# Performance work log

Measured on AMD Instinct MI355X. Metric: run time of the kernel, lower is better.

## Reference

```python
import jax, jax.numpy as jnp
import numpy as np

N_HEAD = 8
EPS_LN = 1e-5
EPS_SM = 1e-16


def _mlp(x, w1, b1, g, beta, w2, b2):
    # Linear -> ReLU -> LayerNorm -> Linear (matches nn.Sequential in torch module)
    h = jax.nn.relu(x @ w1 + b1)
    mu = jnp.mean(h, axis=-1, keepdims=True)
    var = jnp.mean((h - mu) ** 2, axis=-1, keepdims=True)
    h = (h - mu) * jax.lax.rsqrt(var + EPS_LN) * g + beta
    return h @ w2 + b2


def setup_inputs() -> dict:
    B, L, D, E, Fe, H = 4, 4096, 128, 262144, 5, N_HEAD
    ks = jax.random.split(jax.random.key(0), 20)
    s = 0.02
    p = lambda i, sh: jax.random.normal(ks[i], sh, jnp.float32) * s
    z = lambda n: jnp.zeros((n,), jnp.float32)
    inp = {
        "key": jax.random.normal(ks[0], (B, L, D), jnp.float32),
        "value": jax.random.normal(ks[1], (B, L, D), jnp.float32),
        "query": jax.random.normal(ks[2], (B, L, D), jnp.float32),
        "edge_feats": jax.random.normal(ks[3], (E, Fe), jnp.float32),
        "atten_masks": jnp.zeros((E,), jnp.float32),  # present in signature, unused in forward
        "batch_indices": jax.random.randint(ks[4], (E,), 0, B),
        "head_indices": jax.random.randint(ks[5], (E,), 0, L),
        "tail_indices": jax.random.randint(ks[6], (E,), 0, L),
        "key_w": p(7, (D, D)), "key_b": z(D),
        "query_w": p(8, (D, D)), "query_b": z(D),
        "value_w": p(9, (D, D)), "value_b": z(D),
        "proj_w": p(10, (D, D)), "proj_b": z(D),
        "ea_w1": p(11, (Fe, D)), "ea_b1": z(D), "ea_g": jnp.ones((D,), jnp.float32), "ea_beta": z(D), "ea_w2": p(12, (D, H)), "ea_b2": z(H),
        "ek_w1": p(13, (Fe, D)), "ek_b1": z(D), "ek_g": jnp.ones((D,), jnp.float32), "ek_beta": z(D), "ek_w2": p(14, (D, D)), "ek_b2": z(D),
        "ev_w1": p(15, (Fe, D)), "ev_b1": z(D), "ev_g": jnp.ones((D,), jnp.float32), "ev_beta": z(D), "ev_w2": p(16, (D, D)), "ev_b2": z(D),
    }
    return inp


def reference(key, value, query, edge_feats, atten_masks,
              batch_indices, head_indices, tail_indices,
              key_w, key_b, query_w, query_b, value_w, value_b, proj_w, proj_b,
              ea_w1, ea_b1, ea_g, ea_beta, ea_w2, ea_b2,
              ek_w1, ek_b1, ek_g, ek_beta, ek_w2, ek_b2,
              ev_w1, ev_b1, ev_g, ev_beta, ev_w2, ev_b2):
    B, L, D = query.shape
    H = N_HEAD
    dh = D // H
    N = B * L
    # node projections -> [B*L, H, dh]
    k = (key @ key_w + key_b).reshape(N, H, dh)
    q = (query @ query_w + query_b).reshape(N, H, dh)
    v = (value @ value_w + value_b).reshape(N, H, dh)
    heads = batch_indices * L + head_indices  # destination node per edge
    tails = batch_indices * L + tail_indices  # source node per edge
    # per-edge gather + edge-conditioned k/v
    qs = q[heads]
    ks = k[tails] + _mlp(edge_feats, ek_w1, ek_b1, ek_g, ek_beta, ek_w2, ek_b2).reshape(-1, H, dh)
    vs = v[tails] + _mlp(edge_feats, ev_w1, ev_b1, ev_g, ev_beta, ev_w2, ev_b2).reshape(-1, H, dh)
    w = jnp.sum(ks * qs, axis=-1) + _mlp(edge_feats, ea_w1, ea_b1, ea_g, ea_beta, ea_w2, ea_b2)  # [E, H]
    # segment softmax over edges grouped by destination node
    m = jax.ops.segment_max(w, heads, num_segments=N)
    ex = jnp.exp(w - m[heads])
    denom = jax.ops.segment_sum(ex, heads, num_segments=N)
    att = ex / (denom[heads] + EPS_SM)  # [E, H]
    # weighted scatter-sum combine
    y = jax.ops.segment_sum(att[:, :, None] * vs, heads, num_segments=N).reshape(B, L, D)
    return y @ proj_w + proj_b
```

## Files before the change

### kernel.cpp

```cpp
#include <hip/hip_runtime.h>
#include <hip/hip_bf16.h>

#define D      128
#define NHEAD  8
#define FE     5
#define LSEQ   4096
#define EPB    64
#define NNODE  16384
#define EPS_LN 1e-5f
#define EPS_SM 1e-16f

typedef unsigned short ushort_t;
typedef __bf16 bf16x8 __attribute__((ext_vector_type(8)));
typedef float  f32x4  __attribute__((ext_vector_type(4)));

__device__ __forceinline__ ushort_t f2bf(float x) {
    __hip_bfloat16 b = __float2bfloat16(x);
    return __builtin_bit_cast(unsigned short, b);
}
__device__ __forceinline__ float bf2f(ushort_t u) {
    __hip_bfloat16 b = __builtin_bit_cast(__hip_bfloat16, u);
    return __bfloat162float(b);
}
__device__ __forceinline__ float i2f(int x)  { return __builtin_bit_cast(float, x); }
__device__ __forceinline__ int   f2i(float x){ return __builtin_bit_cast(int, x); }

union Pk8 { ushort_t u[8]; uint4 v; };

__global__ __launch_bounds__(256) void pre_kernel(
    const float* __restrict__ ekw2, const float* __restrict__ evw2,
    const float* __restrict__ eaw2,
    const float* __restrict__ kw, const float* __restrict__ qw,
    const float* __restrict__ vw,
    ushort_t* __restrict__ eksw, ushort_t* __restrict__ evsw, ushort_t* __restrict__ easw,
    ushort_t* __restrict__ kwsw, ushort_t* __restrict__ qwsw, ushort_t* __restrict__ vwsw,
    const int* __restrict__ bidx, const int* __restrict__ hidx,
    int* __restrict__ cnt, int E)
{
    const int t = threadIdx.x;
    if (blockIdx.x < 41) {
        const int g = blockIdx.x * 256 + t;
        const float* src; ushort_t* dst; int frag, ncols = 128, nvalid = 128;
        if (g < 2048)       { src = ekw2; dst = eksw; frag = g; }
        else if (g < 4096)  { src = evw2; dst = evsw; frag = g - 2048; }
        else if (g < 4352)  { src = eaw2; dst = easw; frag = g - 4096; ncols = 8; nvalid = 8; }
        else if (g < 6400)  { src = kw;   dst = kwsw; frag = g - 4352; }
        else if (g < 8448)  { src = qw;   dst = qwsw; frag = g - 6400; }
        else if (g < 10496) { src = vw;   dst = vwsw; frag = g - 8448; }
        else return;
        const int s = (frag >> 6) & 3;
        const int l = frag & 63;
        const int n = ((frag >> 8) << 4) + (l & 15);
        Pk8 pk;
        #pragma unroll
        for (int j = 0; j < 8; ++j) {
            const int k = s * 32 + (l >> 4) * 8 + j;
            const float v = (n < nvalid) ? src[k * ncols + n] : 0.f;
            pk.u[j] = f2bf(v);
        }
        *(uint4*)(dst + (size_t)frag * 8) = pk.v;
        return;
    }
    const int e = (blockIdx.x - 41) * 256 + t;
    if (e < E) atomicAdd(&cnt[bidx[e] * LSEQ + hidx[e]], 1);
}

__global__ __launch_bounds__(1024) void scan16k(
    const int* __restrict__ cnt, int* __restrict__ base)
{
    __shared__ int part[1024];
    const int t = threadIdx.x;
    int v[16], ex[16], s = 0;
    #pragma unroll
    for (int i = 0; i < 16; ++i) v[i] = cnt[t * 16 + i];
    #pragma unroll
    for (int i = 0; i < 16; ++i) { ex[i] = s; s += v[i]; }
    part[t] = s;
    __syncthreads();
    for (int off = 1; off < 1024; off <<= 1) {
        const int x = (t >= off) ? part[t - off] : 0;
        __syncthreads();
        part[t] += x;
        __syncthreads();
    }
    const int boff = (t > 0) ? part[t - 1] : 0;
    #pragma unroll
    for (int i = 0; i < 16; ++i) base[t * 16 + i] = boff + ex[i];
    if (t == 1023) base[NNODE] = boff + s;
}

__global__ __launch_bounds__(256) void mid_kernel(
    const float* __restrict__ key, const float* __restrict__ value,
    const float* __restrict__ query,
    const float* __restrict__ key_b, const float* __restrict__ value_b,
    const float* __restrict__ query_b,
    const ushort_t* __restrict__ kwsw, const ushort_t* __restrict__ vwsw,
    const ushort_t* __restrict__ qwsw,
    ushort_t* __restrict__ k16, ushort_t* __restrict__ v16, ushort_t* __restrict__ q16,
    const int* __restrict__ bidx, const int* __restrict__ hidx, const int* __restrict__ tidx,
    const float* __restrict__ edge_feats,
    const int* __restrict__ base, int* __restrict__ cnt, float* __restrict__ rec,
    int nqm, int E)
{
    const int t  = threadIdx.x;
    const int nq = 3 * nqm;
    if ((int)blockIdx.x < nq) {
        const int which = blockIdx.x / nqm;
        const int blk   = blockIdx.x % nqm;
        const float* X     = (which == 0) ? key   : (which == 1) ? value   : query;
        const float* bias  = (which == 0) ? key_b : (which == 1) ? value_b : query_b;
        const ushort_t* Ww = (which == 0) ? kwsw  : (which == 1) ? vwsw    : qwsw;
        ushort_t* Y        = (which == 0) ? k16   : (which == 1) ? v16     : q16;

        const int mt    = t >> 6;
        const int l     = t & 63;
        const int rbase = blk * 64 + mt * 16;
        const int colb  = l & 15;
        const int row0  = (l >> 4) * 4;
        const int arow  = rbase + colb;
        const int koff  = (l >> 4) * 8;

        bf16x8 afr[4];
        #pragma unroll
        for (int s = 0; s < 4; ++s) {
            const float4 x0 = *(const float4*)&X[(size_t)arow * D + s * 32 + koff];
            const float4 x1 = *(const float4*)&X[(size_t)arow * D + s * 32 + koff + 4];
            Pk8 p8;
            p8.u[0] = f2bf(x0.x); p8.u[1] = f2bf(x0.y);
            p8.u[2] = f2bf(x0.z); p8.u[3] = f2bf(x0.w);
            p8.u[4] = f2bf(x1.x); p8.u[5] = f2bf(x1.y);
            p8.u[6] = f2bf(x1.z); p8.u[7] = f2bf(x1.w);
            afr[s] = __builtin_bit_cast(bf16x8, p8.v);
        }
        #pragma unroll
        for (int nt = 0; nt < 8; ++nt) {
            f32x4 acc = {0.f, 0.f, 0.f, 0.f};
            #pragma unroll
            for (int s = 0; s < 4; ++s) {
                const bf16x8 bfr = *(const bf16x8*)(Ww + (size_t)((nt * 4 + s) * 64 + l) * 8);
                acc = __builtin_amdgcn_mfma_f32_16x16x32_bf16(afr[s], bfr, acc, 0, 0, 0);
            }
            const int col = nt * 16 + colb;
            const float b = bias[col];
            #pragma unroll
            for (int r = 0; r < 4; ++r)
                Y[(size_t)(rbase + row0 + r) * D + col] = f2bf(acc[r] + b);
        }
        return;
    }

    const int e = (blockIdx.x - nq) * 256 + t;
    if (e >= E) return;
    const int bb = bidx[e];
    const int nh = bb * LSEQ + hidx[e];
    const int nt = bb * LSEQ + tidx[e];
    const int slot = atomicSub(&cnt[nh], 1) - 1;
    const int p = base[nh] + slot;
    float ef[FE];
    #pragma unroll
    for (int f = 0; f < FE; ++f) ef[f] = edge_feats[(size_t)e * FE + f];
    *(float4*)&rec[(size_t)p * 8]     = float4{ef[0], ef[1], ef[2], ef[3]};
    *(float4*)&rec[(size_t)p * 8 + 4] = float4{ef[4], i2f(nh), i2f(nt), 0.f};
}

__global__ __launch_bounds__(256, 4) void edge_kernel(
    const float* __restrict__ rec,
    const float* __restrict__ ea_w1, const float* __restrict__ ea_b1,
    const float* __restrict__ ea_g,  const float* __restrict__ ea_be, const float* __restrict__ ea_b2,
    const float* __restrict__ ek_w1, const float* __restrict__ ek_b1,
    const float* __restrict__ ek_g,  const float* __restrict__ ek_be, const float* __restrict__ ek_b2,
    const float* __restrict__ ev_w1, const float* __restrict__ ev_b1,
    const float* __restrict__ ev_g,  const float* __restrict__ ev_be, const float* __restrict__ ev_b2,
    const ushort_t* __restrict__ easw, const ushort_t* __restrict__ eksw, const ushort_t* __restrict__ evsw,
    const ushort_t* __restrict__ k16, const ushort_t* __restrict__ q16, const ushort_t* __restrict__ v16,
    float* __restrict__ ex_ws, ushort_t* __restrict__ vs_ws)
{
    __shared__ float pw1[3][FE * D];
    __shared__ float pb1[3][D], pg[3][D], pbe[3][D];
    __shared__ float pb2k[D], pb2v[D], pb2a[NHEAD];
    __shared__ float ef_s[EPB][FE];
    __shared__ int   eh_s[EPB], et_s[EPB];

    const int t   = threadIdx.x;
    const int e0g = blockIdx.x * EPB;

    for (int i = t; i < FE * D; i += 256) { pw1[0][i] = ea_w1[i]; pw1[1][i] = ek_w1[i]; pw1[2][i] = ev_w1[i]; }
    if (t < D) {
        pb1[0][t] = ea_b1[t]; pb1[1][t] = ek_b1[t]; pb1[2][t] = ev_b1[t];
        pg [0][t] = ea_g [t]; pg [1][t] = ek_g [t]; pg [2][t] = ev_g [t];
        pbe[0][t] = ea_be[t]; pbe[1][t] = ek_be[t]; pbe[2][t] = ev_be[t];
        pb2k[t] = ek_b2[t];   pb2v[t] = ev_b2[t];
        if (t < NHEAD) pb2a[t] = ea_b2[t];
    }
    if (t < 128) {
        const int pl = t >> 1, half = t & 1;
        const float4 v = *(const float4*)&rec[((size_t)e0g + pl) * 8 + half * 4];
        if (half == 0) {
            ef_s[pl][0] = v.x; ef_s[pl][1] = v.y; ef_s[pl][2] = v.z; ef_s[pl][3] = v.w;
        } else {
            ef_s[pl][4] = v.x; eh_s[pl] = f2i(v.y); et_s[pl] = f2i(v.z);
        }
    }
    __syncthreads();

    const int mt   = t >> 6;
    const int l    = t & 63;
    const int qt   = l & 3;
    const int per  = l >> 2;
    const int row0 = (l >> 4) * 4;
    const int colb = l & 15;
    const int src  = 4 * colb + (l >> 4);
    const int bsrc = (l & 48);

    int tn[4], hnn[4];
    #pragma unroll
    for (int r = 0; r < 4; ++r) { tn[r] = et_s[mt*16 + row0 + r]; hnn[r] = eh_s[mt*16 + row0 + r]; }

    float efr[FE];
    #pragma unroll
    for (int f = 0; f < FE; ++f) efr[f] = ef_s[mt*16 + per][f];

    auto first_layer = [&](int m, uint4 pk[4]) {
        const float4* w1v = (const float4*)&pw1[m][0];
        const float4* b1v = (const float4*)&pb1[m][0];
        const float4* gv  = (const float4*)&pg[m][0];
        const float4* bev = (const float4*)&pbe[m][0];
        float4 hv[4][2];
        float s1 = 0.f, s2 = 0.f;
        #pragma unroll
        for (int s = 0; s < 4; ++s) {
            #pragma unroll
            for (int hc = 0; hc < 2; ++hc) {
                const int idx = s * 8 + qt * 2 + hc;
                float4 a = b1v[idx];
                #pragma unroll
                for (int f = 0; f < FE; ++f) {
                    const float sc = efr[f];
                    const float4 w = w1v[f * 32 + idx];
                    a.x = fmaf(sc, w.x, a.x); a.y = fmaf(sc, w.y, a.y);
                    a.z = fmaf(sc, w.z, a.z); a.w = fmaf(sc, w.w, a.w);
                }
                a.x = fmaxf(a.x, 0.f); a.y = fmaxf(a.y, 0.f);
                a.z = fmaxf(a.z, 0.f); a.w = fmaxf(a.w, 0.f);
                hv[s][hc] = a;
                s1 += a.x + a.y + a.z + a.w;
                s2 += a.x*a.x + a.y*a.y + a.z*a.z + a.w*a.w;
            }
        }
        s1 += __shfl_xor(s1, 1); s1 += __shfl_xor(s1, 2);
        s2 += __shfl_xor(s2, 1); s2 += __shfl_xor(s2, 2);
        const float mu = s1 * (1.f / 128.f);
        const float rs = rsqrtf(s2 * (1.f / 128.f) - mu * mu + EPS_LN);
        #pragma unroll
        for (int s = 0; s < 4; ++s) {
            const int idx = s * 8 + qt * 2;
            const float4 x0 = hv[s][0], x1 = hv[s][1];
            const float4 g0 = gv[idx], g1 = gv[idx + 1];
            const float4 b0 = bev[idx], b1 = bev[idx + 1];
            Pk8 p8;
            p8.u[0] = f2bf(fmaf((x0.x - mu) * rs, g0.x, b0.x));
            p8.u[1] = f2bf(fmaf((x0.y - mu) * rs, g0.y, b0.y));
            p8.u[2] = f2bf(fmaf((x0.z - mu) * rs, g0.z, b0.z));
            p8.u[3] = f2bf(fmaf((x0.w - mu) * rs, g0.w, b0.w));
            p8.u[4] = f2bf(fmaf((x1.x - mu) * rs, g1.x, b1.x));
            p8.u[5] = f2bf(fmaf((x1.y - mu) * rs, g1.y, b1.y));
            p8.u[6] = f2bf(fmaf((x1.z - mu) * rs, g1.z, b1.z));
            p8.u[7] = f2bf(fmaf((x1.w - mu) * rs, g1.w, b1.w));
            pk[s] = p8.v;
        }
    };

    auto gather_afr = [&](const uint4 pk[4], bf16x8 afr[4]) {
        #pragma unroll
        for (int s = 0; s < 4; ++s) {
            uint4 w;
            w.x = (unsigned)__shfl((int)pk[s].x, src);
            w.y = (unsigned)__shfl((int)pk[s].y, src);
            w.z = (unsigned)__shfl((int)pk[s].z, src);
            w.w = (unsigned)__shfl((int)pk[s].w, src);
            afr[s] = __builtin_bit_cast(bf16x8, w);
        }
    };

    uint4 pk[4];
    bf16x8 afr[4];

    float eaacc[4];
    first_layer(0, pk);
    gather_afr(pk, afr);
    {
        f32x4 acc = {0.f, 0.f, 0.f, 0.f};
        #pragma unroll
        for (int s = 0; s < 4; ++s) {
            const bf16x8 bfr = *(const bf16x8*)(easw + (size_t)(s * 64 + l) * 8);
            acc = __builtin_amdgcn_mfma_f32_16x16x32_bf16(afr[s], bfr, acc, 0, 0, 0);
        }
        #pragma unroll
        for (int r = 0; r < 4; ++r) eaacc[r] = acc[r];
    }

    first_layer(1, pk);
    gather_afr(pk, afr);
    #pragma unroll
    for (int nt = 0; nt < NHEAD; ++nt) {
        f32x4 acc = {0.f, 0.f, 0.f, 0.f};
        #pragma unroll
        for (int s = 0; s < 4; ++s) {
            const bf16x8 bfr = *(const bf16x8*)(eksw + (size_t)((nt * 4 + s) * 64 + l) * 8);
            acc = __builtin_amdgcn_mfma_f32_16x16x32_bf16(afr[s], bfr, acc, 0, 0, 0);
        }
        const int col = nt * 16 + colb;
        const float b2 = pb2k[col];
        const float ba = pb2a[nt];
        float pr[4];
        #pragma unroll
        for (int r = 0; r < 4; ++r)
            pr[r] = (acc[r] + b2 + bf2f(k16[(size_t)tn[r] * D + col]))
                    * bf2f(q16[(size_t)hnn[r] * D + col]);
        #pragma unroll
        for (int m = 1; m < 16; m <<= 1) {
            #pragma unroll
            for (int r = 0; r < 4; ++r) pr[r] += __shfl_xor(pr[r], m);
        }
        #pragma unroll
        for (int r = 0; r < 4; ++r) {
            const float ea = __shfl(eaacc[r], bsrc | nt);
            const float ex = __expf(pr[r] + ea + ba);
            if (colb == nt)
                ex_ws[(size_t)(e0g + mt*16 + row0 + r) * NHEAD + nt] = ex;
        }
    }

    first_layer(2, pk);
    gather_afr(pk, afr);
    #pragma unroll
    for (int nt = 0; nt < NHEAD; ++nt) {
        f32x4 acc = {0.f, 0.f, 0.f, 0.f};
        #pragma unroll
        for (int s = 0; s < 4; ++s) {
            const bf16x8 bfr = *(const bf16x8*)(evsw + (size_t)((nt * 4 + s) * 64 + l) * 8);
            acc = __builtin_amdgcn_mfma_f32_16x16x32_bf16(afr[s], bfr, acc, 0, 0, 0);
        }
        const int col = nt * 16 + colb;
        const float b2 = pb2v[col];
        #pragma unroll
        for (int r = 0; r < 4; ++r) {
            const float vs = acc[r] + b2 + bf2f(v16[(size_t)tn[r] * D + col]);
            vs_ws[(size_t)(e0g + mt*16 + row0 + r) * D + col] = f2bf(vs);
        }
    }
}

__global__ __launch_bounds__(512) void agg_out(
    const int* __restrict__ base,
    const float* __restrict__ ex_ws, const ushort_t* __restrict__ vs_ws,
    const float* __restrict__ W, const float* __restrict__ bias,
    float* __restrict__ out)
{
    __shared__ float xs[D][20];
    const int t  = threadIdx.x;
    const int rg = t >> 7;
    const int j  = t & 127;
    const int h  = j >> 4;
    const int n0 = blockIdx.x * 16;

    #pragma unroll
    for (int ni = 0; ni < 4; ++ni) {
        const int n  = n0 + rg * 4 + ni;
        const int s0 = base[n], s1 = base[n + 1];
        float acc = 0.f, den = 0.f;
        int p = s0;
        for (; p + 4 <= s1; p += 4) {
            float ex4[4], vs4[4];
            #pragma unroll
            for (int r = 0; r < 4; ++r) {
                ex4[r] = ex_ws[(size_t)(p + r) * NHEAD + h];
                vs4[r] = bf2f(vs_ws[(size_t)(p + r) * D + j]);
            }
            #pragma unroll
            for (int r = 0; r < 4; ++r) {
                den += ex4[r];
                acc = fmaf(ex4[r], vs4[r], acc);
            }
        }
        for (; p < s1; ++p) {
            const float ex = ex_ws[(size_t)p * NHEAD + h];
            den += ex;
            acc = fmaf(ex, bf2f(vs_ws[(size_t)p * D + j]), acc);
        }
        xs[j][rg * 4 + ni] = acc / (den + EPS_SM);
    }
    __syncthreads();

    float acc[4];
    const float b = bias[j];
    #pragma unroll
    for (int r = 0; r < 4; ++r) acc[r] = b;
    #pragma unroll 4
    for (int i = 0; i < D; ++i) {
        const float w = W[i * D + j];
        const float4 y4 = *(const float4*)&xs[i][rg * 4];
        acc[0] = fmaf(y4.x, w, acc[0]); acc[1] = fmaf(y4.y, w, acc[1]);
        acc[2] = fmaf(y4.z, w, acc[2]); acc[3] = fmaf(y4.w, w, acc[3]);
    }
    #pragma unroll
    for (int r = 0; r < 4; ++r)
        out[(size_t)(n0 + rg * 4 + r) * D + j] = acc[r];
}

extern "C" void kernel_launch(void* const* d_in, const int* in_sizes, int n_in,
                              void* d_out, int out_size, void* d_ws, size_t ws_size,
                              hipStream_t stream)
{
    const float* key        = (const float*)d_in[0];
    const float* value      = (const float*)d_in[1];
    const float* query      = (const float*)d_in[2];
    const float* edge_feats = (const float*)d_in[3];
    const int*   bidx       = (const int*)d_in[5];
    const int*   hidx       = (const int*)d_in[6];
    const int*   tidx       = (const int*)d_in[7];
    const float* key_w   = (const float*)d_in[8];  const float* key_b   = (const float*)d_in[9];
    const float* query_w = (const float*)d_in[10]; const float* query_b = (const float*)d_in[11];
    const float* value_w = (const float*)d_in[12]; const float* value_b = (const float*)d_in[13];
    const float* proj_w  = (const float*)d_in[14]; const float* proj_b  = (const float*)d_in[15];

    const int N = in_sizes[0] / D;
    const int E = in_sizes[5];

    char* ws = (char*)d_ws;
    ushort_t* k16   = (ushort_t*)ws; ws += (size_t)N * D * 2;
    ushort_t* q16   = (ushort_t*)ws; ws += (size_t)N * D * 2;
    ushort_t* v16   = (ushort_t*)ws; ws += (size_t)N * D * 2;
    float* ex_ws    = (float*)ws;    ws += (size_t)E * NHEAD * 4;
    ushort_t* vs_ws = (ushort_t*)ws; ws += (size_t)E * D * 2;
    float* rec      = (float*)ws;    ws += (size_t)E * 8 * 4;
    ushort_t* eksw  = (ushort_t*)ws; ws += (size_t)2048 * 8 * 2;
    ushort_t* evsw  = (ushort_t*)ws; ws += (size_t)2048 * 8 * 2;
    ushort_t* easw  = (ushort_t*)ws; ws += (size_t)256 * 8 * 2;
    ushort_t* kwsw  = (ushort_t*)ws; ws += (size_t)2048 * 8 * 2;
    ushort_t* qwsw  = (ushort_t*)ws; ws += (size_t)2048 * 8 * 2;
    ushort_t* vwsw  = (ushort_t*)ws; ws += (size_t)2048 * 8 * 2;
    int* base = (int*)ws;  ws += (size_t)(N + 1) * 4;
    int* cnt  = (int*)ws;  ws += (size_t)N * 4;

    const int nqm   = N / 64;
    const int nhist = (E + 255) / 256;

    hipMemsetAsync(cnt, 0, (size_t)N * 4, stream);

    pre_kernel<<<41 + nhist, 256, 0, stream>>>(
        (const float*)d_in[26], (const float*)d_in[32], (const float*)d_in[20],
        key_w, query_w, value_w,
        eksw, evsw, easw, kwsw, qwsw, vwsw,
        bidx, hidx, cnt, E);

    scan16k<<<1, 1024, 0, stream>>>(cnt, base);

    mid_kernel<<<3 * nqm + nhist, 256, 0, stream>>>(
        key, value, query,
        key_b, value_b, query_b,
        kwsw, vwsw, qwsw,
        k16, v16, q16,
        bidx, hidx, tidx, edge_feats,
        base, cnt, rec, nqm, E);

    edge_kernel<<<E / EPB, 256, 0, stream>>>(
        rec,
        (const float*)d_in[16], (const float*)d_in[17], (const float*)d_in[18],
        (const float*)d_in[19], (const float*)d_in[21],
        (const float*)d_in[22], (const float*)d_in[23], (const float*)d_in[24],
        (const float*)d_in[25], (const float*)d_in[27],
        (const float*)d_in[28], (const float*)d_in[29], (const float*)d_in[30],
        (const float*)d_in[31], (const float*)d_in[33],
        easw, eksw, evsw,
        k16, q16, v16,
        ex_ws, vs_ws);

    agg_out<<<N / 16, 512, 0, stream>>>(base, ex_ws, vs_ws, proj_w, proj_b, (float*)d_out);
}
```

Measured before the change: 296.2 us.

## Compute edge MLP first layer with split-bf16 MFMA instead of scalar FMAs

The first Linear layer of the three edge MLPs (5 inputs to 128 neurons plus bias) moves from per-thread fp32 FMA loops over shared-memory weights to MFMA 16x16x32 bf16 ops. Weights are pre-swizzled in pre_kernel into hi/lo bf16 pairs, with the bias folded in through constant-one inputs, which keeps near-fp32 accuracy. The LayerNorm output is now staged through a padded shared-memory tile to form the A fragments for the second layer, replacing the shuffle-based gather. It frees VALU work and shared memory for weights, at the cost of an extra LDS round trip and a small pre-processing step.

```diff
diff --git a/kernel.cpp b/kernel.cpp
--- a/kernel.cpp
+++ b/kernel.cpp
@@ -32,36 +32,66 @@
     const float* __restrict__ eaw2,
     const float* __restrict__ kw, const float* __restrict__ qw,
     const float* __restrict__ vw,
+    const float* __restrict__ eaw1, const float* __restrict__ eab1,
+    const float* __restrict__ ekw1, const float* __restrict__ ekb1,
+    const float* __restrict__ evw1, const float* __restrict__ evb1,
     ushort_t* __restrict__ eksw, ushort_t* __restrict__ evsw, ushort_t* __restrict__ easw,
     ushort_t* __restrict__ kwsw, ushort_t* __restrict__ qwsw, ushort_t* __restrict__ vwsw,
+    ushort_t* __restrict__ w1fg,
     const int* __restrict__ bidx, const int* __restrict__ hidx,
     int* __restrict__ cnt, int E)
 {
     const int t = threadIdx.x;
-    if (blockIdx.x < 41) {
+    if (blockIdx.x < 47) {
         const int g = blockIdx.x * 256 + t;
-        const float* src; ushort_t* dst; int frag, ncols = 128, nvalid = 128;
-        if (g < 2048)       { src = ekw2; dst = eksw; frag = g; }
-        else if (g < 4096)  { src = evw2; dst = evsw; frag = g - 2048; }
-        else if (g < 4352)  { src = eaw2; dst = easw; frag = g - 4096; ncols = 8; nvalid = 8; }
-        else if (g < 6400)  { src = kw;   dst = kwsw; frag = g - 4352; }
-        else if (g < 8448)  { src = qw;   dst = qwsw; frag = g - 6400; }
-        else if (g < 10496) { src = vw;   dst = vwsw; frag = g - 8448; }
-        else return;
-        const int s = (frag >> 6) & 3;
-        const int l = frag & 63;
-        const int n = ((frag >> 8) << 4) + (l & 15);
+        if (g < 10496) {
+            const float* src; ushort_t* dst; int frag, ncols = 128, nvalid = 128;
+            if (g < 2048)       { src = ekw2; dst = eksw; frag = g; }
+            else if (g < 4096)  { src = evw2; dst = evsw; frag = g - 2048; }
+            else if (g < 4352)  { src = eaw2; dst = easw; frag = g - 4096; ncols = 8; nvalid = 8; }
+            else if (g < 6400)  { src = kw;   dst = kwsw; frag = g - 4352; }
+            else if (g < 8448)  { src = qw;   dst = qwsw; frag = g - 6400; }
+            else                { src = vw;   dst = vwsw; frag = g - 8448; }
+            const int s = (frag >> 6) & 3;
+            const int l = frag & 63;
+            const int n = ((frag >> 8) << 4) + (l & 15);
+            Pk8 pk;
+            #pragma unroll
+            for (int j = 0; j < 8; ++j) {
+                const int k = s * 32 + (l >> 4) * 8 + j;
+                const float v = (n < nvalid) ? src[k * ncols + n] : 0.f;
+                pk.u[j] = f2bf(v);
+            }
+            *(uint4*)(dst + (size_t)frag * 8) = pk.v;
+            return;
+        }
+        const int g2  = g - 10496;
+        const int mlp = g2 >> 9;
+        const int q   = g2 & 511;
+        const int mt  = q >> 6;
+        const int l   = q & 63;
+        const int mi  = l & 15;
+        const int gk  = l >> 4;
+        const float* w1 = (mlp == 0) ? eaw1 : (mlp == 1) ? ekw1 : evw1;
+        const float* b1 = (mlp == 0) ? eab1 : (mlp == 1) ? ekb1 : evb1;
+        const int neuron = mt * 16 + mi;
         Pk8 pk;
         #pragma unroll
         for (int j = 0; j < 8; ++j) {
-            const int k = s * 32 + (l >> 4) * 8 + j;
-            const float v = (n < nvalid) ? src[k * ncols + n] : 0.f;
-            pk.u[j] = f2bf(v);
-        }
-        *(uint4*)(dst + (size_t)frag * 8) = pk.v;
+            const int kf = gk * 8 + j;
+            float v = 0.f; bool lo = false;
+            if (kf < FE)                            v = w1[kf * D + neuron];
+            else if (kf >= 8  && kf < 8  + FE)      v = w1[(kf - 8) * D + neuron];
+            else if (kf >= 16 && kf < 16 + FE)    { v = w1[(kf - 16) * D + neuron]; lo = true; }
+            else if (kf == 24)                      v = b1[neuron];
+            else if (kf == 25)                    { v = b1[neuron]; lo = true; }
+            const ushort_t hi = f2bf(v);
+            pk.u[j] = lo ? f2bf(v - bf2f(hi)) : hi;
+        }
+        *(uint4*)(w1fg + (size_t)g2 * 8) = pk.v;
         return;
     }
-    const int e = (blockIdx.x - 41) * 256 + t;
+    const int e = (blockIdx.x - 47) * 256 + t;
     if (e < E) atomicAdd(&cnt[bidx[e] * LSEQ + hidx[e]], 1);
 }
 
@@ -165,18 +195,16 @@
 
 __global__ __launch_bounds__(256, 4) void edge_kernel(
     const float* __restrict__ rec,
-    const float* __restrict__ ea_w1, const float* __restrict__ ea_b1,
+    const ushort_t* __restrict__ w1fg,
     const float* __restrict__ ea_g,  const float* __restrict__ ea_be, const float* __restrict__ ea_b2,
-    const float* __restrict__ ek_w1, const float* __restrict__ ek_b1,
     const float* __restrict__ ek_g,  const float* __restrict__ ek_be, const float* __restrict__ ek_b2,
-    const float* __restrict__ ev_w1, const float* __restrict__ ev_b1,
     const float* __restrict__ ev_g,  const float* __restrict__ ev_be, const float* __restrict__ ev_b2,
     const ushort_t* __restrict__ easw, const ushort_t* __restrict__ eksw, const ushort_t* __restrict__ evsw,
     const ushort_t* __restrict__ k16, const ushort_t* __restrict__ q16, const ushort_t* __restrict__ v16,
     float* __restrict__ ex_ws, ushort_t* __restrict__ vs_ws)
 {
-    __shared__ float pw1[3][FE * D];
-    __shared__ float pb1[3][D], pg[3][D], pbe[3][D];
+    __shared__ ushort_t hn[4][16][136];
+    __shared__ float pg[3][D], pbe[3][D];
     __shared__ float pb2k[D], pb2v[D], pb2a[NHEAD];
     __shared__ float ef_s[EPB][FE];
     __shared__ int   eh_s[EPB], et_s[EPB];
@@ -184,9 +212,7 @@
     const int t   = threadIdx.x;
     const int e0g = blockIdx.x * EPB;
 
-    for (int i = t; i < FE * D; i += 256) { pw1[0][i] = ea_w1[i]; pw1[1][i] = ek_w1[i]; pw1[2][i] = ev_w1[i]; }
     if (t < D) {
-        pb1[0][t] = ea_b1[t]; pb1[1][t] = ek_b1[t]; pb1[2][t] = ev_b1[t];
         pg [0][t] = ea_g [t]; pg [1][t] = ek_g [t]; pg [2][t] = ev_g [t];
         pbe[0][t] = ea_be[t]; pbe[1][t] = ek_be[t]; pbe[2][t] = ev_be[t];
         pb2k[t] = ek_b2[t];   pb2v[t] = ev_b2[t];
@@ -205,89 +231,81 @@
 
     const int mt   = t >> 6;
     const int l    = t & 63;
-    const int qt   = l & 3;
-    const int per  = l >> 2;
-    const int row0 = (l >> 4) * 4;
+    const int h4   = l >> 4;
+    const int row0 = h4 * 4;
     const int colb = l & 15;
-    const int src  = 4 * colb + (l >> 4);
     const int bsrc = (l & 48);
 
     int tn[4], hnn[4];
     #pragma unroll
     for (int r = 0; r < 4; ++r) { tn[r] = et_s[mt*16 + row0 + r]; hnn[r] = eh_s[mt*16 + row0 + r]; }
 
-    float efr[FE];
-    #pragma unroll
-    for (int f = 0; f < FE; ++f) efr[f] = ef_s[mt*16 + per][f];
-
-    auto first_layer = [&](int m, uint4 pk[4]) {
-        const float4* w1v = (const float4*)&pw1[m][0];
-        const float4* b1v = (const float4*)&pb1[m][0];
-        const float4* gv  = (const float4*)&pg[m][0];
-        const float4* bev = (const float4*)&pbe[m][0];
-        float4 hv[4][2];
+    bf16x8 xfr;
+    {
+        const float* e = ef_s[mt * 16 + colb];
+        Pk8 xf;
+        if (h4 == 3) {
+            const ushort_t one = f2bf(1.f);
+            xf.u[0] = one; xf.u[1] = one;
+            #pragma unroll
+            for (int j = 2; j < 8; ++j) xf.u[j] = 0;
+        } else {
+            #pragma unroll
+            for (int f = 0; f < FE; ++f) {
+                const float v = e[f];
+                const ushort_t hi = f2bf(v);
+                xf.u[f] = (h4 == 1) ? f2bf(v - bf2f(hi)) : hi;
+            }
+            xf.u[5] = 0; xf.u[6] = 0; xf.u[7] = 0;
+        }
+        xfr = __builtin_bit_cast(bf16x8, xf.v);
+    }
+
+    ushort_t* hnrow = &hn[mt][colb][0];
+
+    auto first_layer = [&](int m, bf16x8 afr[4]) {
+        const f32x4 zero = {0.f, 0.f, 0.f, 0.f};
+        f32x4 acc[8];
+        #pragma unroll
+        for (int mtile = 0; mtile < 8; ++mtile) {
+            const bf16x8 aw = *(const bf16x8*)(w1fg + (size_t)((m * 8 + mtile) * 64 + l) * 8);
+            acc[mtile] = __builtin_amdgcn_mfma_f32_16x16x32_bf16(aw, xfr, zero, 0, 0, 0);
+        }
         float s1 = 0.f, s2 = 0.f;
         #pragma unroll
-        for (int s = 0; s < 4; ++s) {
-            #pragma unroll
-            for (int hc = 0; hc < 2; ++hc) {
-                const int idx = s * 8 + qt * 2 + hc;
-                float4 a = b1v[idx];
-                #pragma unroll
-                for (int f = 0; f < FE; ++f) {
-                    const float sc = efr[f];
-                    const float4 w = w1v[f * 32 + idx];
-                    a.x = fmaf(sc, w.x, a.x); a.y = fmaf(sc, w.y, a.y);
-                    a.z = fmaf(sc, w.z, a.z); a.w = fmaf(sc, w.w, a.w);
-                }
-                a.x = fmaxf(a.x, 0.f); a.y = fmaxf(a.y, 0.f);
-                a.z = fmaxf(a.z, 0.f); a.w = fmaxf(a.w, 0.f);
-                hv[s][hc] = a;
-                s1 += a.x + a.y + a.z + a.w;
-                s2 += a.x*a.x + a.y*a.y + a.z*a.z + a.w*a.w;
-            }
-        }
-        s1 += __shfl_xor(s1, 1); s1 += __shfl_xor(s1, 2);
-        s2 += __shfl_xor(s2, 1); s2 += __shfl_xor(s2, 2);
+        for (int mtile = 0; mtile < 8; ++mtile) {
+            #pragma unroll
+            for (int r = 0; r < 4; ++r) {
+                const float v = fmaxf(acc[mtile][r], 0.f);
+                acc[mtile][r] = v;
+                s1 += v; s2 += v * v;
+            }
+        }
+        s1 += __shfl_xor(s1, 16); s1 += __shfl_xor(s1, 32);
+        s2 += __shfl_xor(s2, 16); s2 += __shfl_xor(s2, 32);
         const float mu = s1 * (1.f / 128.f);
         const float rs = rsqrtf(s2 * (1.f / 128.f) - mu * mu + EPS_LN);
         #pragma unroll
-        for (int s = 0; s < 4; ++s) {
-            const int idx = s * 8 + qt * 2;
-            const float4 x0 = hv[s][0], x1 = hv[s][1];
-            const float4 g0 = gv[idx], g1 = gv[idx + 1];
-            const float4 b0 = bev[idx], b1 = bev[idx + 1];
-            Pk8 p8;
-            p8.u[0] = f2bf(fmaf((x0.x - mu) * rs, g0.x, b0.x));
-            p8.u[1] = f2bf(fmaf((x0.y - mu) * rs, g0.y, b0.y));
-            p8.u[2] = f2bf(fmaf((x0.z - mu) * rs, g0.z, b0.z));
-            p8.u[3] = f2bf(fmaf((x0.w - mu) * rs, g0.w, b0.w));
-            p8.u[4] = f2bf(fmaf((x1.x - mu) * rs, g1.x, b1.x));
-            p8.u[5] = f2bf(fmaf((x1.y - mu) * rs, g1.y, b1.y));
-            p8.u[6] = f2bf(fmaf((x1.z - mu) * rs, g1.z, b1.z));
-            p8.u[7] = f2bf(fmaf((x1.w - mu) * rs, g1.w, b1.w));
-            pk[s] = p8.v;
-        }
+        for (int mtile = 0; mtile < 8; ++mtile) {
+            const int n0 = mtile * 16 + 4 * h4;
+            const float4 g4 = *(const float4*)&pg[m][n0];
+            const float4 b4 = *(const float4*)&pbe[m][n0];
+            uint2 w;
+            w.x = (unsigned)f2bf(fmaf((acc[mtile][0] - mu) * rs, g4.x, b4.x))
+                | ((unsigned)f2bf(fmaf((acc[mtile][1] - mu) * rs, g4.y, b4.y)) << 16);
+            w.y = (unsigned)f2bf(fmaf((acc[mtile][2] - mu) * rs, g4.z, b4.z))
+                | ((unsigned)f2bf(fmaf((acc[mtile][3] - mu) * rs, g4.w, b4.w)) << 16);
+            *(uint2*)&hnrow[n0] = w;
+        }
+        #pragma unroll
+        for (int s = 0; s < 4; ++s)
+            afr[s] = *(const bf16x8*)&hnrow[32 * s + 8 * h4];
     };
 
-    auto gather_afr = [&](const uint4 pk[4], bf16x8 afr[4]) {
-        #pragma unroll
-        for (int s = 0; s < 4; ++s) {
-            uint4 w;
-            w.x = (unsigned)__shfl((int)pk[s].x, src);
-            w.y = (unsigned)__shfl((int)pk[s].y, src);
-            w.z = (unsigned)__shfl((int)pk[s].z, src);
-            w.w = (unsigned)__shfl((int)pk[s].w, src);
-            afr[s] = __builtin_bit_cast(bf16x8, w);
-        }
-    };
-
-    uint4 pk[4];
     bf16x8 afr[4];
 
     float eaacc[4];
-    first_layer(0, pk);
-    gather_afr(pk, afr);
+    first_layer(0, afr);
     {
         f32x4 acc = {0.f, 0.f, 0.f, 0.f};
         #pragma unroll
@@ -299,8 +317,7 @@
         for (int r = 0; r < 4; ++r) eaacc[r] = acc[r];
     }
 
-    first_layer(1, pk);
-    gather_afr(pk, afr);
+    first_layer(1, afr);
     #pragma unroll
     for (int nt = 0; nt < NHEAD; ++nt) {
         f32x4 acc = {0.f, 0.f, 0.f, 0.f};
@@ -331,8 +348,7 @@
         }
     }
 
-    first_layer(2, pk);
-    gather_afr(pk, afr);
+    first_layer(2, afr);
     #pragma unroll
     for (int nt = 0; nt < NHEAD; ++nt) {
         f32x4 acc = {0.f, 0.f, 0.f, 0.f};
@@ -440,6 +456,7 @@
     ushort_t* kwsw  = (ushort_t*)ws; ws += (size_t)2048 * 8 * 2;
     ushort_t* qwsw  = (ushort_t*)ws; ws += (size_t)2048 * 8 * 2;
     ushort_t* vwsw  = (ushort_t*)ws; ws += (size_t)2048 * 8 * 2;
+    ushort_t* w1fg  = (ushort_t*)ws; ws += (size_t)1536 * 8 * 2;
     int* base = (int*)ws;  ws += (size_t)(N + 1) * 4;
     int* cnt  = (int*)ws;  ws += (size_t)N * 4;
 
@@ -448,10 +465,13 @@
 
     hipMemsetAsync(cnt, 0, (size_t)N * 4, stream);
 
-    pre_kernel<<<41 + nhist, 256, 0, stream>>>(
+    pre_kernel<<<47 + nhist, 256, 0, stream>>>(
         (const float*)d_in[26], (const float*)d_in[32], (const float*)d_in[20],
         key_w, query_w, value_w,
-        eksw, evsw, easw, kwsw, qwsw, vwsw,
+        (const float*)d_in[16], (const float*)d_in[17],
+        (const float*)d_in[22], (const float*)d_in[23],
+        (const float*)d_in[28], (const float*)d_in[29],
+        eksw, evsw, easw, kwsw, qwsw, vwsw, w1fg,
         bidx, hidx, cnt, E);
 
     scan16k<<<1, 1024, 0, stream>>>(cnt, base);
@@ -465,13 +485,10 @@
         base, cnt, rec, nqm, E);
 
     edge_kernel<<<E / EPB, 256, 0, stream>>>(
-        rec,
-        (const float*)d_in[16], (const float*)d_in[17], (const float*)d_in[18],
-        (const float*)d_in[19], (const float*)d_in[21],
-        (const float*)d_in[22], (const float*)d_in[23], (const float*)d_in[24],
-        (const float*)d_in[25], (const float*)d_in[27],
-        (const float*)d_in[28], (const float*)d_in[29], (const float*)d_in[30],
-        (const float*)d_in[31], (const float*)d_in[33],
+        rec, w1fg,
+        (const float*)d_in[18], (const float*)d_in[19], (const float*)d_in[21],
+        (const float*)d_in[24], (const float*)d_in[25], (const float*)d_in[27],
+        (const float*)d_in[30], (const float*)d_in[31], (const float*)d_in[33],
         easw, eksw, evsw,
         k16, q16, v16,
         ex_ws, vs_ws);
```

After: 410.7 us. +38.7%, slower.
